# Optimization experiments

Hardware: AMD Instinct MI355X
Metric: run time of the kernel (lower is better)

The kernel has to match this reference:

```python
import jax, jax.numpy as jnp
import numpy as np

NUM_KNOTS = 256
DEGREE = 3
NUM_BASIS = NUM_KNOTS - DEGREE - 1  # 252
N = 1_048_576


def setup_inputs() -> dict:
    key = jax.random.key(0)
    # evaluation points in [-pi, pi), shape [N, 1] like the torch module
    x = jax.random.uniform(key, (N, 1), jnp.float32, -np.pi, np.pi)
    # knot vector: constant buffer from __init__
    knots = jnp.linspace(-np.pi, np.pi, NUM_KNOTS, dtype=jnp.float32)
    return {"x": x, "knots": knots}


def reference(x, knots):
    """Cox-de Boor B-spline basis, computed bottom-up (dynamic programming).

    Mathematically identical to the naive recursion in the torch module:
    same indicator base case ([knots[j], knots[j+1])) and same denominator>0
    guards, but each level is computed once and fully vectorized over N and j.
    """
    xs = x[:, 0]  # [N]
    # degree-0 basis: indicator of half-open knot interval -> [N, K-1]
    B = ((knots[:-1] <= xs[:, None]) & (xs[:, None] < knots[1:])).astype(jnp.float32)
    for k in range(1, DEGREE + 1):
        m = NUM_KNOTS - 1 - k  # number of basis functions at level k
        d1 = knots[k:k + m] - knots[:m]          # knots[j+k]   - knots[j]
        d2 = knots[k + 1:k + 1 + m] - knots[1:1 + m]  # knots[j+k+1] - knots[j+1]
        w1 = jnp.where(d1 > 0, (xs[:, None] - knots[:m]) / jnp.where(d1 > 0, d1, 1.0), 0.0)
        w2 = jnp.where(d2 > 0, (knots[k + 1:k + 1 + m] - xs[:, None]) / jnp.where(d2 > 0, d2, 1.0), 0.0)
        B = w1 * B[:, :m] + w2 * B[:, 1:1 + m]
    # level DEGREE already has exactly NUM_BASIS columns
    return B[:, :NUM_BASIS]
```

## Files before the change

### kernel.cpp

```cpp
#include <hip/hip_runtime.h>


constexpr int NUM_KNOTS = 256;
constexpr int NUM_BASIS = 252;
constexpr int CHUNKS    = 63;
constexpr int TROWS     = 32;
constexpr int TILE_F4   = TROWS * CHUNKS;
constexpr int BLOCK     = 256;

typedef float f4 __attribute__((ext_vector_type(4)));

__global__ __launch_bounds__(BLOCK) void bspline_kernel(
    const float* __restrict__ X, const float* __restrict__ knots,
    float* __restrict__ out, int n, int ntiles)
{
    __shared__ float s_knots[NUM_KNOTS];
    __shared__ f4    s_img[TILE_F4];

    const int tid = threadIdx.x;
    s_knots[tid] = knots[tid];
    for (int i = tid; i < TILE_F4; i += BLOCK) s_img[i] = (f4)0.0f;
    __syncthreads();

    int  prev_clo   = 0;
    bool prev_valid = false;

    for (int tile = blockIdx.x; tile < ntiles; tile += gridDim.x) {
        const int tbase = tile * TROWS;

        if (tid < TROWS) {
            const int row = tbase + tid;
            float x    = X[min(row, n - 1)];
            float k0   = s_knots[0];
            float kend = s_knots[NUM_KNOTS - 1];
            float inv_h = (float)(NUM_KNOTS - 1) / (kend - k0);

            int j0 = (int)floorf((x - k0) * inv_h);
            j0 = min(max(j0, 0), NUM_KNOTS - 2);
            while (j0 > 0 && x < s_knots[j0]) --j0;
            while (j0 < NUM_KNOTS - 2 && x >= s_knots[j0 + 1]) ++j0;

            float cb[4] = {1.0f, 0.0f, 0.0f, 0.0f};
            #pragma unroll
            for (int k = 1; k <= 3; ++k) {
                #pragma unroll
                for (int i = 3; i >= 0; --i) {
                    if (i > k) continue;
                    int j = j0 - k + i;
                    float plo = (i >= 1)     ? cb[i - 1] : 0.0f;
                    float phi = (i <= k - 1) ? cb[i]     : 0.0f;
                    float val = 0.0f;
                    if (j >= 0 && j <= NUM_KNOTS - 2 - k) {
                        float kj  = s_knots[j];
                        float kj1 = s_knots[j + 1];
                        float kjk = s_knots[j + k];
                        float kk1 = s_knots[j + k + 1];
                        val = (x - kj) / (kjk - kj) * plo
                            + (kk1 - x) / (kk1 - kj1) * phi;
                    }
                    cb[i] = val;
                }
            }

            int s = j0 - 3;
            int a = s & 3;
            int clo = s >> 2;
            float lo0=cb[0], lo1=cb[1], lo2=cb[2], lo3=cb[3];
            float hi0=0.f, hi1=0.f, hi2=0.f, hi3=0.f;
            if (a & 2) { hi3=hi1; hi2=hi0; hi1=lo3; hi0=lo2;
                         lo3=lo1; lo2=lo0; lo1=0.f; lo0=0.f; }
            if (a & 1) { hi3=hi2; hi2=hi1; hi1=hi0; hi0=lo3;
                         lo3=lo2; lo2=lo1; lo1=lo0; lo0=0.f; }
            f4 vlo; vlo.x=lo0; vlo.y=lo1; vlo.z=lo2; vlo.w=lo3;
            f4 vhi; vhi.x=hi0; vhi.y=hi1; vhi.z=hi2; vhi.w=hi3;

            f4* rowimg = s_img + tid * CHUNKS;
            f4  z = (f4)0.0f;
            if (prev_valid) {
                if (prev_clo >= 0)          rowimg[prev_clo]     = z;
                if (prev_clo < CHUNKS - 1)  rowimg[prev_clo + 1] = z;
            }
            if (row < n) {
                if (clo >= 0)          rowimg[clo]     = vlo;
                if (clo < CHUNKS - 1)  rowimg[clo + 1] = vhi;
                prev_clo = clo; prev_valid = true;
            } else {
                prev_valid = false;
            }
        }
        __syncthreads();

        f4* dst = (f4*)out + (size_t)tbase * CHUNKS;
        if (tbase + TROWS <= n) {
            #pragma unroll
            for (int i = 0; i < 7; ++i)
                dst[tid + 256 * i] = s_img[tid + 256 * i];
            if (tid < TILE_F4 - 7 * 256)
                dst[tid + 7 * 256] = s_img[tid + 7 * 256];
        } else {
            int lim = (n - tbase) * CHUNKS;
            for (int i = tid; i < lim; i += BLOCK) dst[i] = s_img[i];
        }
        __syncthreads();
    }
}

extern "C" void kernel_launch(void* const* d_in, const int* in_sizes, int n_in,
                              void* d_out, int out_size, void* d_ws, size_t ws_size,
                              hipStream_t stream) {
    const float* x     = (const float*)d_in[0];
    const float* knots = (const float*)d_in[1];
    float* out = (float*)d_out;
    int n = in_sizes[0];
    int ntiles = (n + TROWS - 1) / TROWS;
    int grid = 1024;
    if (grid > ntiles) grid = ntiles;
    bspline_kernel<<<grid, BLOCK, 0, stream>>>(x, knots, out, n, ntiles);
}
```

Baseline: 227.5 us.

## Double-buffer shared tile image to overlap basis compute with global stores

Uses two LDS tile images so the next tile's Cox-de Boor evaluation and band writes run while the current tile is streamed to global memory, leaving one barrier per tile instead of two. The first barrier uses a manual lgkmcnt wait and a raw s_barrier. Tiles are now assigned to blocks as contiguous ranges, and the grid drops from 1024 to 512 blocks. This doubles LDS use per block and halves the block count, which may cut the occupancy available to hide store latency in a kernel bound by write bandwidth.

Result: no change. 229.9 us (+1.1%).

```diff
diff --git a/kernel.cpp b/kernel.cpp
--- a/kernel.cpp
+++ b/kernel.cpp
@@ -10,98 +10,125 @@
 
 typedef float f4 __attribute__((ext_vector_type(4)));
 
+__device__ __forceinline__ void cox_de_boor(float x, const float* sk,
+                                            int& clo_out, f4& vlo_out, f4& vhi_out)
+{
+    float k0 = sk[0], kend = sk[NUM_KNOTS - 1];
+    float inv_h = (float)(NUM_KNOTS - 1) / (kend - k0);
+    int j0 = (int)floorf((x - k0) * inv_h);
+    j0 = min(max(j0, 0), NUM_KNOTS - 2);
+    while (j0 > 0 && x < sk[j0]) --j0;
+    while (j0 < NUM_KNOTS - 2 && x >= sk[j0 + 1]) ++j0;
+
+    float cb[4] = {1.0f, 0.0f, 0.0f, 0.0f};
+    #pragma unroll
+    for (int k = 1; k <= 3; ++k) {
+        #pragma unroll
+        for (int i = 3; i >= 0; --i) {
+            if (i > k) continue;
+            int j = j0 - k + i;
+            float plo = (i >= 1)     ? cb[i - 1] : 0.0f;
+            float phi = (i <= k - 1) ? cb[i]     : 0.0f;
+            float val = 0.0f;
+            if (j >= 0 && j <= NUM_KNOTS - 2 - k) {
+                float kj  = sk[j];
+                float kj1 = sk[j + 1];
+                float kjk = sk[j + k];
+                float kk1 = sk[j + k + 1];
+                val = (x - kj) / (kjk - kj) * plo
+                    + (kk1 - x) / (kk1 - kj1) * phi;
+            }
+            cb[i] = val;
+        }
+    }
+
+    int s = j0 - 3, a = s & 3, clo = s >> 2;
+    float lo0=cb[0], lo1=cb[1], lo2=cb[2], lo3=cb[3];
+    float hi0=0.f, hi1=0.f, hi2=0.f, hi3=0.f;
+    if (a & 2) { hi3=hi1; hi2=hi0; hi1=lo3; hi0=lo2;
+                 lo3=lo1; lo2=lo0; lo1=0.f; lo0=0.f; }
+    if (a & 1) { hi3=hi2; hi2=hi1; hi1=hi0; hi0=lo3;
+                 lo3=lo2; lo2=lo1; lo1=lo0; lo0=0.f; }
+    f4 vlo; vlo.x=lo0; vlo.y=lo1; vlo.z=lo2; vlo.w=lo3;
+    f4 vhi; vhi.x=hi0; vhi.y=hi1; vhi.z=hi2; vhi.w=hi3;
+    clo_out = clo; vlo_out = vlo; vhi_out = vhi;
+}
+
+__device__ __forceinline__ void write_band(f4* img, int lane, int& prev,
+                                           bool valid, int clo, f4 vlo, f4 vhi)
+{
+    f4* rowimg = img + lane * CHUNKS;
+    f4 z = (f4)0.0f;
+    if (prev > -99) {
+        if (prev >= 0)          rowimg[prev]     = z;
+        if (prev < CHUNKS - 1)  rowimg[prev + 1] = z;
+    }
+    if (valid) {
+        if (clo >= 0)           rowimg[clo]      = vlo;
+        if (clo < CHUNKS - 1)   rowimg[clo + 1]  = vhi;
+        prev = clo;
+    } else {
+        prev = -100;
+    }
+}
+
 __global__ __launch_bounds__(BLOCK) void bspline_kernel(
     const float* __restrict__ X, const float* __restrict__ knots,
-    float* __restrict__ out, int n, int ntiles)
+    float* __restrict__ out, int n, int ntiles, int K)
 {
     __shared__ float s_knots[NUM_KNOTS];
-    __shared__ f4    s_img[TILE_F4];
+    __shared__ f4    imgA[TILE_F4];
+    __shared__ f4    imgB[TILE_F4];
 
-    const int tid = threadIdx.x;
+    const int tid  = threadIdx.x;
+    const int t0   = blockIdx.x * K;
+    const int tend = min(t0 + K, ntiles);
+    if (t0 >= tend) return;
+
     s_knots[tid] = knots[tid];
-    for (int i = tid; i < TILE_F4; i += BLOCK) s_img[i] = (f4)0.0f;
+    for (int i = tid; i < TILE_F4; i += BLOCK) { imgA[i] = (f4)0.0f; imgB[i] = (f4)0.0f; }
     __syncthreads();
 
-    int  prev_clo   = 0;
-    bool prev_valid = false;
+    int prevA = -100, prevB = -100;
 
-    for (int tile = blockIdx.x; tile < ntiles; tile += gridDim.x) {
-        const int tbase = tile * TROWS;
+    if (tid < TROWS) {
+        int row = t0 * TROWS + tid;
+        float x = X[min(row, n - 1)];
+        int clo; f4 vlo, vhi;
+        cox_de_boor(x, s_knots, clo, vlo, vhi);
+        write_band(imgA, tid, prevA, row < n, clo, vlo, vhi);
+    }
+    asm volatile("s_waitcnt lgkmcnt(0)" ::: "memory");
+    __builtin_amdgcn_s_barrier();
 
-        if (tid < TROWS) {
-            const int row = tbase + tid;
-            float x    = X[min(row, n - 1)];
-            float k0   = s_knots[0];
-            float kend = s_knots[NUM_KNOTS - 1];
-            float inv_h = (float)(NUM_KNOTS - 1) / (kend - k0);
+    for (int t = t0; t < tend; ++t) {
+        const bool curA = ((t - t0) & 1) == 0;
+        const f4* cur = curA ? imgA : imgB;
 
-            int j0 = (int)floorf((x - k0) * inv_h);
-            j0 = min(max(j0, 0), NUM_KNOTS - 2);
-            while (j0 > 0 && x < s_knots[j0]) --j0;
-            while (j0 < NUM_KNOTS - 2 && x >= s_knots[j0 + 1]) ++j0;
-
-            float cb[4] = {1.0f, 0.0f, 0.0f, 0.0f};
-            #pragma unroll
-            for (int k = 1; k <= 3; ++k) {
-                #pragma unroll
-                for (int i = 3; i >= 0; --i) {
-                    if (i > k) continue;
-                    int j = j0 - k + i;
-                    float plo = (i >= 1)     ? cb[i - 1] : 0.0f;
-                    float phi = (i <= k - 1) ? cb[i]     : 0.0f;
-                    float val = 0.0f;
-                    if (j >= 0 && j <= NUM_KNOTS - 2 - k) {
-                        float kj  = s_knots[j];
-                        float kj1 = s_knots[j + 1];
-                        float kjk = s_knots[j + k];
-                        float kk1 = s_knots[j + k + 1];
-                        val = (x - kj) / (kjk - kj) * plo
-                            + (kk1 - x) / (kk1 - kj1) * phi;
-                    }
-                    cb[i] = val;
-                }
-            }
-
-            int s = j0 - 3;
-            int a = s & 3;
-            int clo = s >> 2;
-            float lo0=cb[0], lo1=cb[1], lo2=cb[2], lo3=cb[3];
-            float hi0=0.f, hi1=0.f, hi2=0.f, hi3=0.f;
-            if (a & 2) { hi3=hi1; hi2=hi0; hi1=lo3; hi0=lo2;
-                         lo3=lo1; lo2=lo0; lo1=0.f; lo0=0.f; }
-            if (a & 1) { hi3=hi2; hi2=hi1; hi1=hi0; hi0=lo3;
-                         lo3=lo2; lo2=lo1; lo1=lo0; lo0=0.f; }
-            f4 vlo; vlo.x=lo0; vlo.y=lo1; vlo.z=lo2; vlo.w=lo3;
-            f4 vhi; vhi.x=hi0; vhi.y=hi1; vhi.z=hi2; vhi.w=hi3;
-
-            f4* rowimg = s_img + tid * CHUNKS;
-            f4  z = (f4)0.0f;
-            if (prev_valid) {
-                if (prev_clo >= 0)          rowimg[prev_clo]     = z;
-                if (prev_clo < CHUNKS - 1)  rowimg[prev_clo + 1] = z;
-            }
-            if (row < n) {
-                if (clo >= 0)          rowimg[clo]     = vlo;
-                if (clo < CHUNKS - 1)  rowimg[clo + 1] = vhi;
-                prev_clo = clo; prev_valid = true;
-            } else {
-                prev_valid = false;
-            }
-        }
-        __syncthreads();
-
+        const int tbase = t * TROWS;
         f4* dst = (f4*)out + (size_t)tbase * CHUNKS;
         if (tbase + TROWS <= n) {
             #pragma unroll
             for (int i = 0; i < 7; ++i)
-                dst[tid + 256 * i] = s_img[tid + 256 * i];
+                dst[tid + 256 * i] = cur[tid + 256 * i];
             if (tid < TILE_F4 - 7 * 256)
-                dst[tid + 7 * 256] = s_img[tid + 7 * 256];
+                dst[tid + 7 * 256] = cur[tid + 7 * 256];
         } else {
             int lim = (n - tbase) * CHUNKS;
-            for (int i = tid; i < lim; i += BLOCK) dst[i] = s_img[i];
+            for (int i = tid; i < lim; i += BLOCK) dst[i] = cur[i];
         }
-        __syncthreads();
+
+        if (t + 1 < tend && tid < TROWS) {
+            int row = (t + 1) * TROWS + tid;
+            float x = X[min(row, n - 1)];
+            int clo; f4 vlo, vhi;
+            cox_de_boor(x, s_knots, clo, vlo, vhi);
+            if (curA) write_band(imgB, tid, prevB, row < n, clo, vlo, vhi);
+            else      write_band(imgA, tid, prevA, row < n, clo, vlo, vhi);
+        }
+
+        asm volatile("s_waitcnt lgkmcnt(0)" ::: "memory");
+        __builtin_amdgcn_s_barrier();
     }
 }
 
@@ -113,7 +140,7 @@
     float* out = (float*)d_out;
     int n = in_sizes[0];
     int ntiles = (n + TROWS - 1) / TROWS;
-    int grid = 1024;
-    if (grid > ntiles) grid = ntiles;
-    bspline_kernel<<<grid, BLOCK, 0, stream>>>(x, knots, out, n, ntiles);
+    int grid = ntiles < 512 ? ntiles : 512;
+    int K = (ntiles + grid - 1) / grid;
+    bspline_kernel<<<grid, BLOCK, 0, stream>>>(x, knots, out, n, ntiles, K);
 }
```
